# Optimization experiments

Hardware: AMD Instinct MI355X
Metric: run time of the kernel (lower is better)

The kernel has to match this reference:

```python
import jax, jax.numpy as jnp
import numpy as np

N = 50000      # nodes
E = 800000     # edges (avg degree 16)
IN, HID, OUT = 128, 256, 64
G = 500        # graphs in the batch (100 nodes each)
NEG_SLOPE = 0.01
EPS = 1e-12


def setup_inputs() -> dict:
    key = jax.random.key(0)
    ks = jax.random.split(key, 9)
    x = jax.random.normal(ks[0], (N, IN), jnp.float32)
    edge_index = jax.random.randint(ks[1], (2, E), 0, N, dtype=jnp.int32)
    # sorted segment ids with every graph present (100 nodes per graph)
    batch = jnp.repeat(jnp.arange(G, dtype=jnp.int32), N // G)
    def lin(k, fan_in, fan_out):
        s = 1.0 / np.sqrt(fan_in)
        kw, kb = jax.random.split(k)
        W = jax.random.uniform(kw, (fan_in, fan_out), jnp.float32, -s, s)
        b = jax.random.uniform(kb, (fan_out,), jnp.float32, -s, s)
        return W, b
    W1, b1 = lin(ks[2], IN, HID)
    W2, b2 = lin(ks[3], HID, HID)
    W3, b3 = lin(ks[4], HID, OUT)
    return {"x": x, "edge_index": edge_index, "batch": batch,
            "W1": W1, "b1": b1, "W2": W2, "b2": b2, "W3": W3, "b3": b3}


def _sage_conv(x, edge_index, W, b):
    # SAGEConv(aggr='add', root_weight=False, normalize=True):
    # gather source features, scatter-add to targets, linear, L2 normalize.
    src, dst = edge_index[0], edge_index[1]
    agg = jax.ops.segment_sum(x[src], dst, num_segments=x.shape[0])  # [N, d_in]
    out = agg @ W + b                                                 # [N, d_out]
    nrm = jnp.linalg.norm(out, axis=-1, keepdims=True)
    return out / jnp.maximum(nrm, EPS)


def reference(x, edge_index, batch, W1, b1, W2, b2, W3, b3):
    h = _sage_conv(x, edge_index, W1, b1)
    h = jax.nn.leaky_relu(h, NEG_SLOPE)          # dropout p=0 -> identity
    h = _sage_conv(h, edge_index, W2, b2)
    h = jax.nn.leaky_relu(h, NEG_SLOPE)
    h = _sage_conv(h, edge_index, W3, b3)
    # get_zero_nodes: first node of each graph (batch sorted, all G present)
    mask = jnp.concatenate([jnp.ones((1,), bool), batch[1:] != batch[:-1]])
    first_idx = jnp.nonzero(mask, size=G)[0]
    return h[first_idx]                          # [G, OUT]
```

## Files before the change

kernel.cpp:

```cpp
#include <hip/hip_runtime.h>

#define N_NODES 50000
#define E_EDGES 800000
#define IN_DIM  128
#define HID_DIM 256
#define OUT_DIM 64
#define G_GRAPHS 500
#define CAP 64
#define NBINS 196
#define BINCAP 5120

typedef __attribute__((ext_vector_type(8))) short short8;
typedef __attribute__((ext_vector_type(4))) float float4v;

__device__ __forceinline__ float bf2f(unsigned short u) {
  union { unsigned int i; float f; } c; c.i = ((unsigned int)u) << 16; return c.f;
}
__device__ __forceinline__ unsigned short f2bf(float f) {
  union { float f; unsigned int i; } c; c.f = f;
  unsigned int x = c.i;
  x += 0x7FFFu + ((x >> 16) & 1u);
  return (unsigned short)(x >> 16);
}
__device__ __forceinline__ unsigned int fbits(float f) {
  union { float f; unsigned int i; } c; c.f = f; return c.i;
}
__device__ __forceinline__ float bits2f(unsigned int u) {
  union { unsigned int i; float f; } c; c.i = u; return c.f;
}


__global__ __launch_bounds__(256) void prep1(
    const int* __restrict__ src, const int* __restrict__ dst,
    const int* __restrict__ batch,
    const float* __restrict__ x,
    const float* __restrict__ W1, const float* __restrict__ W2,
    unsigned int* __restrict__ binbuf, int* __restrict__ bin_next,
    int* __restrict__ first_node, unsigned char* __restrict__ is_first,
    unsigned short* __restrict__ xb,
    unsigned short* __restrict__ W1t, unsigned short* __restrict__ W2t) {
  const int b = blockIdx.x, tid = threadIdx.x;
  if (b < 200) {
    __shared__ int cnt[NBINS];
    __shared__ int gbase[NBINS];
    for (int i = tid; i < NBINS; i += 256) cnt[i] = 0;
    __syncthreads();
    const int base = b * 4096;
    unsigned int pk[16]; int bp[16];
#pragma unroll
    for (int u = 0; u < 16; ++u) {
      const int e = base + u * 256 + tid;
      bp[u] = -1;
      if (e < E_EDGES) {
        const int d = dst[e];
        const int s = src[e];
        const int bin = d >> 8;
        const int pos = atomicAdd(&cnt[bin], 1);
        pk[u] = ((unsigned int)(d & 255) << 16) | (unsigned int)s;
        bp[u] = (bin << 16) | pos;
      }
    }
    __syncthreads();
    for (int i = tid; i < NBINS; i += 256)
      gbase[i] = atomicAdd(&bin_next[i], cnt[i]);
    __syncthreads();
#pragma unroll
    for (int u = 0; u < 16; ++u) {
      if (bp[u] >= 0) {
        const int bin = bp[u] >> 16, pos = bp[u] & 0xFFFF;
        const int idx = gbase[bin] + pos;
        if (idx < BINCAP) binbuf[bin * BINCAP + idx] = pk[u];
      }
    }
  } else if (b < 6450) {
    const int t = (b - 200) * 256 + tid;
    const int i = t * 4;
    const float4 v = *(const float4*)(x + i);
    ushort4 u;
    u.x = f2bf(v.x); u.y = f2bf(v.y); u.z = f2bf(v.z); u.w = f2bf(v.w);
    *(ushort4*)(xb + i) = u;
    if (t < N_NODES) {
      const int fl = (t == 0 || batch[t] != batch[t - 1]) ? 1 : 0;
      is_first[t] = (unsigned char)fl;
      if (fl) first_node[batch[t]] = t;
    }
  } else {
    const int t = (b - 6450) * 256 + tid;
    if (t < 8192) {
      const int n = t >> 5, k0 = (t & 31) * 4;
      ushort4 o;
      o.x = f2bf(W1[(k0 + 0) * 256 + n]);
      o.y = f2bf(W1[(k0 + 1) * 256 + n]);
      o.z = f2bf(W1[(k0 + 2) * 256 + n]);
      o.w = f2bf(W1[(k0 + 3) * 256 + n]);
      *(ushort4*)&W1t[n * 128 + k0] = o;
    } else {
      const int v2 = t - 8192;
      const int n = v2 >> 6, k0 = (v2 & 63) * 4;
      ushort4 o;
      o.x = f2bf(W2[(k0 + 0) * 256 + n]);
      o.y = f2bf(W2[(k0 + 1) * 256 + n]);
      o.z = f2bf(W2[(k0 + 2) * 256 + n]);
      o.w = f2bf(W2[(k0 + 3) * 256 + n]);
      *(ushort4*)&W2t[n * 256 + k0] = o;
    }
  }
}


__global__ __launch_bounds__(512) void prep2(
    const unsigned int* __restrict__ binbuf, const int* __restrict__ bin_next,
    const unsigned char* __restrict__ is_first,
    int* __restrict__ deg, unsigned short* __restrict__ srcs,
    int* __restrict__ list2, int* __restrict__ cnt2) {
  __shared__ unsigned short img[256 * CAP];
  __shared__ int cnt[256];
  const int tid = threadIdx.x;
  const int bin = blockIdx.x;
  if (tid < 256) cnt[tid] = 0;
  __syncthreads();
  const int total = min(bin_next[bin], BINCAP);
  const unsigned int* bb = binbuf + bin * BINCAP;
  for (int i = tid; i < total; i += 512) {
    const unsigned int pk = bb[i];
    const int nl = pk >> 16;
    const int pos = atomicAdd(&cnt[nl], 1);
    if (pos < CAP) img[(nl << 6) + pos] = (unsigned short)(pk & 0xFFFFu);
  }
  __syncthreads();
  const int node0 = bin << 8;
  const int nend = min(N_NODES, node0 + 256);
  if (tid < 256 && node0 + tid < nend) {
    const int c = min(cnt[tid], CAP);
    deg[node0 + tid] = cnt[tid];
    if (is_first[node0 + tid]) {
      const int base = atomicAdd(cnt2, c);
      for (int q = 0; q < c; ++q) list2[base + q] = (int)img[(tid << 6) + q];
    }
  }
  const int nwords = (nend - node0) * 32;
  unsigned int* dstw = (unsigned int*)(srcs + ((size_t)node0 << 6));
  const unsigned int* srcw = (const unsigned int*)img;
  for (int i = tid; i < nwords; i += 512) dstw[i] = srcw[i];
}


template<int K, bool LIST>
__global__ __launch_bounds__(512, 8) void fused_layer(
    const unsigned short* __restrict__ H,
    const int* __restrict__ deg, const unsigned short* __restrict__ srcs,
    const unsigned short* __restrict__ Wt,
    const float* __restrict__ bias,
    unsigned short* __restrict__ Hout,
    const int* __restrict__ nodelist,
    const int* __restrict__ pcount)
{
  constexpr int M = 256;
  constexpr int TN = 16;
  constexpr int VPT = K / 64;
  constexpr int LDK = K + 8;
  __shared__ unsigned short a_hi[TN][LDK];
  __shared__ unsigned short a_lo[TN][LDK];
  __shared__ float ssq_tot[TN];
  __shared__ int nid_s[TN];
  const int tid = threadIdx.x;
  const int lane = tid & 63;
  const int wv = tid >> 6;

  int total = N_NODES;
  if constexpr (LIST) {
    total = __builtin_amdgcn_readfirstlane(*pcount);
    if (blockIdx.x * TN >= total) return;
  }

  if (tid < TN) {
    int gi = blockIdx.x * TN + tid;
    if constexpr (LIST) {
      if (gi >= total) gi = total - 1;
      nid_s[tid] = nodelist[gi];
    } else {
      nid_s[tid] = gi;
    }
    ssq_tot[tid] = 0.f;
  }
  __syncthreads();

  const unsigned short* hb = H + lane * VPT;
  const int node0 = __builtin_amdgcn_readfirstlane(nid_s[2 * wv]);
  const int node1 = __builtin_amdgcn_readfirstlane(nid_s[2 * wv + 1]);
  const int cnt0 = __builtin_amdgcn_readfirstlane(min(deg[node0], CAP));
  const int cnt1 = __builtin_amdgcn_readfirstlane(min(deg[node1], CAP));
  int idx0 = 0, idx1 = 0;
  if (lane < cnt0) idx0 = srcs[(node0 << 6) + lane];
  if (lane < cnt1) idx1 = srcs[(node1 << 6) + lane];

  float acc0[VPT], acc1[VPT];
#pragma unroll
  for (int q = 0; q < VPT; ++q) { acc0[q] = 0.f; acc1[q] = 0.f; }
  int j0 = 0, j1 = 0;

  if constexpr (VPT == 2) {
    while (j0 + 16 <= cnt0 && j1 + 16 <= cnt1) {
      int s0[16], s1[16];
#pragma unroll
      for (int u = 0; u < 16; ++u) {
        s0[u] = __builtin_amdgcn_readlane(idx0, j0 + u);
        s1[u] = __builtin_amdgcn_readlane(idx1, j1 + u);
      }
      ushort2 r0[16], r1[16];
#pragma unroll
      for (int u = 0; u < 16; ++u) r0[u] = *(const ushort2*)(hb + s0[u] * K);
#pragma unroll
      for (int u = 0; u < 16; ++u) r1[u] = *(const ushort2*)(hb + s1[u] * K);
#pragma unroll
      for (int u = 0; u < 16; ++u) {
        acc0[0] += bf2f(r0[u].x); acc0[1] += bf2f(r0[u].y);
        acc1[0] += bf2f(r1[u].x); acc1[1] += bf2f(r1[u].y);
      }
      j0 += 16; j1 += 16;
    }
  }

#pragma unroll
  for (int i = 0; i < 2; ++i) {
    const int nn = 2 * wv + i;
    const int cnt = i ? cnt1 : cnt0;
    const int idx = i ? idx1 : idx0;
    float (&acc)[VPT] = i ? acc1 : acc0;
    int j = i ? j1 : j0;

    for (; j + 16 <= cnt; j += 16) {
      int s[16];
#pragma unroll
      for (int u = 0; u < 16; ++u) s[u] = __builtin_amdgcn_readlane(idx, j + u);
      if constexpr (VPT == 4) {
        ushort4 r[16];
#pragma unroll
        for (int u = 0; u < 16; ++u) r[u] = *(const ushort4*)(hb + s[u] * K);
#pragma unroll
        for (int u = 0; u < 16; ++u) {
          acc[0] += bf2f(r[u].x); acc[1] += bf2f(r[u].y);
          acc[2] += bf2f(r[u].z); acc[3] += bf2f(r[u].w);
        }
      } else {
        ushort2 r[16];
#pragma unroll
        for (int u = 0; u < 16; ++u) r[u] = *(const ushort2*)(hb + s[u] * K);
#pragma unroll
        for (int u = 0; u < 16; ++u) {
          acc[0] += bf2f(r[u].x); acc[1] += bf2f(r[u].y);
        }
      }
    }
    for (; j < cnt; j += 8) {
      int s[8]; float w[8];
#pragma unroll
      for (int u = 0; u < 8; ++u) {
        const int q = j + u;
        const int qm = (q < cnt) ? q : (cnt - 1);
        s[u] = __builtin_amdgcn_readlane(idx, qm);
        w[u] = (q < cnt) ? 1.f : 0.f;
      }
      if constexpr (VPT == 4) {
        ushort4 r[8];
#pragma unroll
        for (int u = 0; u < 8; ++u) r[u] = *(const ushort4*)(hb + s[u] * K);
#pragma unroll
        for (int u = 0; u < 8; ++u) {
          acc[0] = fmaf(w[u], bf2f(r[u].x), acc[0]);
          acc[1] = fmaf(w[u], bf2f(r[u].y), acc[1]);
          acc[2] = fmaf(w[u], bf2f(r[u].z), acc[2]);
          acc[3] = fmaf(w[u], bf2f(r[u].w), acc[3]);
        }
      } else {
        ushort2 r[8];
#pragma unroll
        for (int u = 0; u < 8; ++u) r[u] = *(const ushort2*)(hb + s[u] * K);
#pragma unroll
        for (int u = 0; u < 8; ++u) {
          acc[0] = fmaf(w[u], bf2f(r[u].x), acc[0]);
          acc[1] = fmaf(w[u], bf2f(r[u].y), acc[1]);
        }
      }
    }

    unsigned short h[VPT], l[VPT];
#pragma unroll
    for (int jj = 0; jj < VPT; ++jj) {
      const unsigned int u = fbits(acc[jj]);
      h[jj] = (unsigned short)(u >> 16);
      const float res = acc[jj] - bits2f(u & 0xFFFF0000u);
      l[jj] = (unsigned short)(fbits(res) >> 16);
    }
    if constexpr (VPT == 4) {
      *(ushort4*)&a_hi[nn][lane * 4] = make_ushort4(h[0], h[1], h[2], h[3]);
      *(ushort4*)&a_lo[nn][lane * 4] = make_ushort4(l[0], l[1], l[2], l[3]);
    } else {
      *(ushort2*)&a_hi[nn][lane * 2] = make_ushort2(h[0], h[1]);
      *(ushort2*)&a_lo[nn][lane * 2] = make_ushort2(l[0], l[1]);
    }
  }
  __syncthreads();

  const int g = lane >> 4;
  const int lc = lane & 15;
  float4v dacc0 = (float4v){0.f, 0.f, 0.f, 0.f};
  float4v dacc1 = (float4v){0.f, 0.f, 0.f, 0.f};
  const unsigned short* W0 = Wt + (size_t)(wv * 16 + lc) * K + g * 8;
  const unsigned short* W1r = Wt + (size_t)((wv + 8) * 16 + lc) * K + g * 8;
#pragma unroll
  for (int ks = 0; ks < K / 32; ++ks) {
    const short8 ah = *(const short8*)&a_hi[lc][ks * 32 + g * 8];
    const short8 al = *(const short8*)&a_lo[lc][ks * 32 + g * 8];
    const short8 b0 = *(const short8*)(W0 + ks * 32);
    const short8 b1 = *(const short8*)(W1r + ks * 32);
    dacc0 = __builtin_amdgcn_mfma_f32_16x16x32_bf16(ah, b0, dacc0, 0, 0, 0);
    dacc0 = __builtin_amdgcn_mfma_f32_16x16x32_bf16(al, b0, dacc0, 0, 0, 0);
    dacc1 = __builtin_amdgcn_mfma_f32_16x16x32_bf16(ah, b1, dacc1, 0, 0, 0);
    dacc1 = __builtin_amdgcn_mfma_f32_16x16x32_bf16(al, b1, dacc1, 0, 0, 0);
  }

  const float bn0 = bias[wv * 16 + lc];
  const float bn1 = bias[(wv + 8) * 16 + lc];
  float4v o0 = dacc0 + bn0;
  float4v o1 = dacc1 + bn1;
  float sq[4];
#pragma unroll
  for (int r = 0; r < 4; ++r) sq[r] = o0[r] * o0[r] + o1[r] * o1[r];
#pragma unroll
  for (int off = 1; off < 16; off <<= 1) {
#pragma unroll
    for (int r = 0; r < 4; ++r) sq[r] += __shfl_xor(sq[r], off);
  }
  if (lc == 0) {
#pragma unroll
    for (int r = 0; r < 4; ++r) atomicAdd(&ssq_tot[g * 4 + r], sq[r]);
  }
  __syncthreads();

#pragma unroll
  for (int r = 0; r < 4; ++r) {
    const float inv = 1.f / fmaxf(sqrtf(ssq_tot[g * 4 + r]), 1e-12f);
    float v0 = o0[r] * inv;
    float v1 = o1[r] * inv;
    v0 = (v0 >= 0.f) ? v0 : 0.01f * v0;
    v1 = (v1 >= 0.f) ? v1 : 0.01f * v1;
    const int nd = nid_s[g * 4 + r];
    Hout[(size_t)nd * M + wv * 16 + lc] = f2bf(v0);
    Hout[(size_t)nd * M + (wv + 8) * 16 + lc] = f2bf(v1);
  }
}


__global__ __launch_bounds__(64) void layer3_kernel(
    const unsigned short* __restrict__ H2,
    const int* __restrict__ deg, const unsigned short* __restrict__ srcs,
    const int* __restrict__ first_node,
    const float* __restrict__ W,
    const float* __restrict__ bias,
    float* __restrict__ out)
{
  __shared__ float a_s[HID_DIM];
  const int g = blockIdx.x;
  const int lane = threadIdx.x;
  const int node = first_node[g];
  const int cnt = min(deg[node], CAP);
  float acc[4] = {0.f, 0.f, 0.f, 0.f};
  for (int p = 0; p < cnt; ++p) {
    const int s = srcs[(node << 6) + p];
    const ushort4 u = *(const ushort4*)(H2 + (size_t)s * HID_DIM + lane * 4);
    acc[0] += bf2f(u.x); acc[1] += bf2f(u.y); acc[2] += bf2f(u.z); acc[3] += bf2f(u.w);
  }
  *(float4*)&a_s[lane * 4] = make_float4(acc[0], acc[1], acc[2], acc[3]);
  __syncthreads();
  float o = bias[lane];
#pragma unroll 8
  for (int k = 0; k < HID_DIM; ++k) o += a_s[k] * W[k * OUT_DIM + lane];
  float ss = o * o;
#pragma unroll
  for (int off = 32; off > 0; off >>= 1) ss += __shfl_xor(ss, off);
  const float inv = 1.f / fmaxf(sqrtf(ss), 1e-12f);
  out[(size_t)g * OUT_DIM + lane] = o * inv;
}


extern "C" void kernel_launch(void* const* d_in, const int* in_sizes, int n_in,
                              void* d_out, int out_size, void* d_ws, size_t ws_size,
                              hipStream_t stream) {
  (void)in_sizes; (void)n_in; (void)out_size; (void)ws_size;
  const float* x   = (const float*)d_in[0];
  const int* ei    = (const int*)d_in[1];
  const int* batch = (const int*)d_in[2];
  const float* W1  = (const float*)d_in[3];
  const float* b1  = (const float*)d_in[4];
  const float* W2  = (const float*)d_in[5];
  const float* b2  = (const float*)d_in[6];
  const float* W3  = (const float*)d_in[7];
  const float* b3  = (const float*)d_in[8];
  const int* src = ei;
  const int* dst = ei + E_EDGES;

  char* ws = (char*)d_ws;
  size_t off = 0;
  auto alloc = [&](size_t bytes) {
    void* p = ws + off;
    off = (off + bytes + 255) & ~(size_t)255;
    return p;
  };
  int* cnts    = (int*)alloc(256);
  int* bin_next= (int*)alloc((size_t)NBINS * 4);
  const size_t zero_len = off;
  int* cnt2 = cnts;

  int* deg    = (int*)alloc((size_t)N_NODES * 4);
  unsigned short* srcs = (unsigned short*)alloc((size_t)N_NODES * CAP * 2);
  int* first  = (int*)alloc((size_t)G_GRAPHS * 4);
  unsigned char* is_first = (unsigned char*)alloc((size_t)N_NODES);
  int* list2  = (int*)alloc((size_t)G_GRAPHS * CAP * 4);
  unsigned int* binbuf = (unsigned int*)alloc((size_t)NBINS * BINCAP * 4);
  unsigned short* W1t = (unsigned short*)alloc((size_t)256 * 128 * 2);
  unsigned short* W2t = (unsigned short*)alloc((size_t)256 * 256 * 2);
  unsigned short* h2 = (unsigned short*)alloc((size_t)N_NODES * HID_DIM * 2);
  unsigned short* xb = h2;
  unsigned short* h1 = (unsigned short*)alloc((size_t)N_NODES * HID_DIM * 2);

  hipMemsetAsync(cnts, 0, zero_len, stream);

  prep1<<<6546, 256, 0, stream>>>(src, dst, batch, x, W1, W2,
                                  binbuf, bin_next, first, is_first, xb, W1t, W2t);
  prep2<<<NBINS, 512, 0, stream>>>(binbuf, bin_next, is_first, deg, srcs, list2, cnt2);

  fused_layer<IN_DIM, false><<<N_NODES / 16, 512, 0, stream>>>(
      xb, deg, srcs, W1t, b1, h1, nullptr, nullptr);
  fused_layer<HID_DIM, true><<<(G_GRAPHS * CAP) / 16, 512, 0, stream>>>(
      h1, deg, srcs, W2t, b2, h2, list2, cnt2);
  layer3_kernel<<<G_GRAPHS, 64, 0, stream>>>(h2, deg, srcs, first, W3, b3, (float*)d_out);
}
```

Before: 197.1 us.

## Replace atomic edge binning with per-block sort and fuse layer-3 aggregation into layer 2

Edge binning no longer uses global atomic bin counters or a memset. Each block sorts its own edge chunk by bin in shared memory and publishes prefix offsets, which prep2 reads back per bin. Layer 2 now runs four blocks per graph over that graph's first-node neighbour slots and writes per-graph partial sums of the activated outputs, so h2 is never stored or re-gathered. Layer 3 only adds the four partials. This removes a memset launch, global atomics and a gather pass, at the cost of a prefix-scan inside prep1 and some idle lanes for padded neighbour slots.

```diff
diff --git a/kernel.cpp b/kernel.cpp
--- a/kernel.cpp
+++ b/kernel.cpp
@@ -8,7 +8,7 @@
 #define G_GRAPHS 500
 #define CAP 64
 #define NBINS 196
-#define BINCAP 5120
+#define NEB   200
 
 typedef __attribute__((ext_vector_type(8))) short short8;
 typedef __attribute__((ext_vector_type(4))) float float4v;
@@ -35,15 +35,18 @@
     const int* __restrict__ batch,
     const float* __restrict__ x,
     const float* __restrict__ W1, const float* __restrict__ W2,
-    unsigned int* __restrict__ binbuf, int* __restrict__ bin_next,
-    int* __restrict__ first_node, unsigned char* __restrict__ is_first,
+    unsigned int* __restrict__ gout,
+    unsigned short* __restrict__ pref,
+    unsigned char* __restrict__ is_first,
     unsigned short* __restrict__ xb,
     unsigned short* __restrict__ W1t, unsigned short* __restrict__ W2t) {
+  __shared__ unsigned int s_sorted[4096];
+  __shared__ int s_cnt[256];
+  __shared__ int s_pa[256];
+  __shared__ int s_pb[256];
   const int b = blockIdx.x, tid = threadIdx.x;
-  if (b < 200) {
-    __shared__ int cnt[NBINS];
-    __shared__ int gbase[NBINS];
-    for (int i = tid; i < NBINS; i += 256) cnt[i] = 0;
+  if (b < NEB) {
+    s_cnt[tid] = 0;
     __syncthreads();
     const int base = b * 4096;
     unsigned int pk[16]; int bp[16];
@@ -55,34 +58,42 @@
         const int d = dst[e];
         const int s = src[e];
         const int bin = d >> 8;
-        const int pos = atomicAdd(&cnt[bin], 1);
+        const int r = atomicAdd(&s_cnt[bin], 1);
         pk[u] = ((unsigned int)(d & 255) << 16) | (unsigned int)s;
-        bp[u] = (bin << 16) | pos;
+        bp[u] = (bin << 16) | r;
       }
     }
     __syncthreads();
-    for (int i = tid; i < NBINS; i += 256)
-      gbase[i] = atomicAdd(&bin_next[i], cnt[i]);
+    const int v = s_cnt[tid];
+    s_pa[tid] = v;
     __syncthreads();
+    for (int st = 1; st < 256; st <<= 1) {
+      const int t = (tid >= st) ? s_pa[tid - st] : 0;
+      __syncthreads();
+      s_pa[tid] += t;
+      __syncthreads();
+    }
+    const int excl = s_pa[tid] - v;
+    s_pb[tid] = excl;
+    pref[(b << 8) + tid] = (unsigned short)excl;
+    __syncthreads();
 #pragma unroll
     for (int u = 0; u < 16; ++u) {
-      if (bp[u] >= 0) {
-        const int bin = bp[u] >> 16, pos = bp[u] & 0xFFFF;
-        const int idx = gbase[bin] + pos;
-        if (idx < BINCAP) binbuf[bin * BINCAP + idx] = pk[u];
-      }
-    }
+      if (bp[u] >= 0)
+        s_sorted[s_pb[bp[u] >> 16] + (bp[u] & 0xFFFF)] = pk[u];
+    }
+    __syncthreads();
+    const int nb = s_pa[255];
+    for (int i = tid; i < nb; i += 256) gout[base + i] = s_sorted[i];
   } else if (b < 6450) {
-    const int t = (b - 200) * 256 + tid;
+    const int t = (b - NEB) * 256 + tid;
     const int i = t * 4;
     const float4 v = *(const float4*)(x + i);
     ushort4 u;
     u.x = f2bf(v.x); u.y = f2bf(v.y); u.z = f2bf(v.z); u.w = f2bf(v.w);
     *(ushort4*)(xb + i) = u;
     if (t < N_NODES) {
-      const int fl = (t == 0 || batch[t] != batch[t - 1]) ? 1 : 0;
-      is_first[t] = (unsigned char)fl;
-      if (fl) first_node[batch[t]] = t;
+      is_first[t] = (t == 0 || batch[t] != batch[t - 1]) ? 1 : 0;
     }
   } else {
     const int t = (b - 6450) * 256 + tid;
@@ -109,33 +120,47 @@
 
 
 __global__ __launch_bounds__(512) void prep2(
-    const unsigned int* __restrict__ binbuf, const int* __restrict__ bin_next,
-    const unsigned char* __restrict__ is_first,
+    const unsigned int* __restrict__ gout, const unsigned short* __restrict__ pref,
+    const int* __restrict__ batch, const unsigned char* __restrict__ is_first,
     int* __restrict__ deg, unsigned short* __restrict__ srcs,
-    int* __restrict__ list2, int* __restrict__ cnt2) {
+    unsigned short* __restrict__ list2, int* __restrict__ l2cnt) {
   __shared__ unsigned short img[256 * CAP];
   __shared__ int cnt[256];
+  __shared__ unsigned short st_s[NEB], ln_s[NEB];
   const int tid = threadIdx.x;
   const int bin = blockIdx.x;
   if (tid < 256) cnt[tid] = 0;
-  __syncthreads();
-  const int total = min(bin_next[bin], BINCAP);
-  const unsigned int* bb = binbuf + bin * BINCAP;
-  for (int i = tid; i < total; i += 512) {
-    const unsigned int pk = bb[i];
-    const int nl = pk >> 16;
-    const int pos = atomicAdd(&cnt[nl], 1);
-    if (pos < CAP) img[(nl << 6) + pos] = (unsigned short)(pk & 0xFFFFu);
+  if (tid < NEB) {
+    const unsigned short a = pref[(tid << 8) + bin];
+    const unsigned short e = pref[(tid << 8) + bin + 1];
+    st_s[tid] = a; ln_s[tid] = (unsigned short)(e - a);
+  }
+  __syncthreads();
+  const int wv = tid >> 6, lane = tid & 63;
+  for (int bb = wv; bb < NEB; bb += 8) {
+    const int len = ln_s[bb];
+    const int go = bb * 4096 + st_s[bb];
+    for (int base = 0; base < len; base += 64) {
+      if (base + lane < len) {
+        const unsigned int pk = gout[go + base + lane];
+        const int nl = pk >> 16;
+        const int pos = atomicAdd(&cnt[nl], 1);
+        if (pos < CAP) img[(nl << 6) + pos] = (unsigned short)(pk & 0xFFFFu);
+      }
+    }
   }
   __syncthreads();
   const int node0 = bin << 8;
   const int nend = min(N_NODES, node0 + 256);
   if (tid < 256 && node0 + tid < nend) {
-    const int c = min(cnt[tid], CAP);
-    deg[node0 + tid] = cnt[tid];
+    const int c = cnt[tid];
+    deg[node0 + tid] = c;
     if (is_first[node0 + tid]) {
-      const int base = atomicAdd(cnt2, c);
-      for (int q = 0; q < c; ++q) list2[base + q] = (int)img[(tid << 6) + q];
+      const int g = batch[node0 + tid];
+      l2cnt[g] = min(c, CAP);
+      unsigned int* d = (unsigned int*)(list2 + g * 64);
+      const unsigned int* s = (const unsigned int*)(img + (tid << 6));
+      for (int q = 0; q < 32; ++q) d[q] = s[q];
     }
   }
   const int nwords = (nend - node0) * 32;
@@ -145,15 +170,16 @@
 }
 
 
-template<int K, bool LIST>
+template<int K, int MODE>
 __global__ __launch_bounds__(512, 8) void fused_layer(
     const unsigned short* __restrict__ H,
     const int* __restrict__ deg, const unsigned short* __restrict__ srcs,
     const unsigned short* __restrict__ Wt,
     const float* __restrict__ bias,
     unsigned short* __restrict__ Hout,
-    const int* __restrict__ nodelist,
-    const int* __restrict__ pcount)
+    const unsigned short* __restrict__ list2,
+    const int* __restrict__ l2cnt,
+    float* __restrict__ agg_part)
 {
   constexpr int M = 256;
   constexpr int TN = 16;
@@ -162,24 +188,23 @@
   __shared__ unsigned short a_hi[TN][LDK];
   __shared__ unsigned short a_lo[TN][LDK];
   __shared__ float ssq_tot[TN];
+  __shared__ float vld_s[TN];
   __shared__ int nid_s[TN];
   const int tid = threadIdx.x;
   const int lane = tid & 63;
   const int wv = tid >> 6;
-
-  int total = N_NODES;
-  if constexpr (LIST) {
-    total = __builtin_amdgcn_readfirstlane(*pcount);
-    if (blockIdx.x * TN >= total) return;
-  }
+  const int graph = blockIdx.x >> 2;
+  const int p = blockIdx.x & 3;
 
   if (tid < TN) {
-    int gi = blockIdx.x * TN + tid;
-    if constexpr (LIST) {
-      if (gi >= total) gi = total - 1;
-      nid_s[tid] = nodelist[gi];
+    if constexpr (MODE == 1) {
+      const int slot = p * 16 + tid;
+      const bool vld = slot < l2cnt[graph];
+      nid_s[tid] = vld ? (int)list2[graph * 64 + slot] : 0;
+      vld_s[tid] = vld ? 1.f : 0.f;
     } else {
-      nid_s[tid] = gi;
+      nid_s[tid] = blockIdx.x * TN + tid;
+      vld_s[tid] = 1.f;
     }
     ssq_tot[tid] = 0.f;
   }
@@ -188,8 +213,12 @@
   const unsigned short* hb = H + lane * VPT;
   const int node0 = __builtin_amdgcn_readfirstlane(nid_s[2 * wv]);
   const int node1 = __builtin_amdgcn_readfirstlane(nid_s[2 * wv + 1]);
-  const int cnt0 = __builtin_amdgcn_readfirstlane(min(deg[node0], CAP));
-  const int cnt1 = __builtin_amdgcn_readfirstlane(min(deg[node1], CAP));
+  int cnt0 = __builtin_amdgcn_readfirstlane(min(deg[node0], CAP));
+  int cnt1 = __builtin_amdgcn_readfirstlane(min(deg[node1], CAP));
+  if constexpr (MODE == 1) {
+    if (vld_s[2 * wv] == 0.f) cnt0 = 0;
+    if (vld_s[2 * wv + 1] == 0.f) cnt1 = 0;
+  }
   int idx0 = 0, idx1 = 0;
   if (lane < cnt0) idx0 = srcs[(node0 << 6) + lane];
   if (lane < cnt1) idx1 = srcs[(node1 << 6) + lane];
@@ -338,24 +367,43 @@
   }
   __syncthreads();
 
-#pragma unroll
-  for (int r = 0; r < 4; ++r) {
-    const float inv = 1.f / fmaxf(sqrtf(ssq_tot[g * 4 + r]), 1e-12f);
-    float v0 = o0[r] * inv;
-    float v1 = o1[r] * inv;
-    v0 = (v0 >= 0.f) ? v0 : 0.01f * v0;
-    v1 = (v1 >= 0.f) ? v1 : 0.01f * v1;
-    const int nd = nid_s[g * 4 + r];
-    Hout[(size_t)nd * M + wv * 16 + lc] = f2bf(v0);
-    Hout[(size_t)nd * M + (wv + 8) * 16 + lc] = f2bf(v1);
+  if constexpr (MODE == 0) {
+#pragma unroll
+    for (int r = 0; r < 4; ++r) {
+      const float inv = 1.f / fmaxf(sqrtf(ssq_tot[g * 4 + r]), 1e-12f);
+      float v0 = o0[r] * inv;
+      float v1 = o1[r] * inv;
+      v0 = (v0 >= 0.f) ? v0 : 0.01f * v0;
+      v1 = (v1 >= 0.f) ? v1 : 0.01f * v1;
+      const int nd = nid_s[g * 4 + r];
+      Hout[(size_t)nd * M + wv * 16 + lc] = f2bf(v0);
+      Hout[(size_t)nd * M + (wv + 8) * 16 + lc] = f2bf(v1);
+    }
+  } else {
+    float s0 = 0.f, s1 = 0.f;
+#pragma unroll
+    for (int r = 0; r < 4; ++r) {
+      const float inv = 1.f / fmaxf(sqrtf(ssq_tot[g * 4 + r]), 1e-12f);
+      float v0 = o0[r] * inv;
+      float v1 = o1[r] * inv;
+      v0 = (v0 >= 0.f) ? v0 : 0.01f * v0;
+      v1 = (v1 >= 0.f) ? v1 : 0.01f * v1;
+      const float w = vld_s[g * 4 + r];
+      s0 += w * v0; s1 += w * v1;
+    }
+    s0 += __shfl_xor(s0, 16); s0 += __shfl_xor(s0, 32);
+    s1 += __shfl_xor(s1, 16); s1 += __shfl_xor(s1, 32);
+    if (lane < 16) {
+      float* pp = agg_part + ((size_t)(graph * 4 + p) << 8);
+      pp[wv * 16 + lane] = s0;
+      pp[128 + wv * 16 + lane] = s1;
+    }
   }
 }
 
 
 __global__ __launch_bounds__(64) void layer3_kernel(
-    const unsigned short* __restrict__ H2,
-    const int* __restrict__ deg, const unsigned short* __restrict__ srcs,
-    const int* __restrict__ first_node,
+    const float* __restrict__ agg_part,
     const float* __restrict__ W,
     const float* __restrict__ bias,
     float* __restrict__ out)
@@ -363,15 +411,12 @@
   __shared__ float a_s[HID_DIM];
   const int g = blockIdx.x;
   const int lane = threadIdx.x;
-  const int node = first_node[g];
-  const int cnt = min(deg[node], CAP);
-  float acc[4] = {0.f, 0.f, 0.f, 0.f};
-  for (int p = 0; p < cnt; ++p) {
-    const int s = srcs[(node << 6) + p];
-    const ushort4 u = *(const ushort4*)(H2 + (size_t)s * HID_DIM + lane * 4);
-    acc[0] += bf2f(u.x); acc[1] += bf2f(u.y); acc[2] += bf2f(u.z); acc[3] += bf2f(u.w);
-  }
-  *(float4*)&a_s[lane * 4] = make_float4(acc[0], acc[1], acc[2], acc[3]);
+  const float* pp = agg_part + ((size_t)g << 10);
+#pragma unroll
+  for (int c = 0; c < 4; ++c) {
+    const int idx = c * 64 + lane;
+    a_s[idx] = pp[idx] + pp[256 + idx] + pp[512 + idx] + pp[768 + idx];
+  }
   __syncthreads();
   float o = bias[lane];
 #pragma unroll 8
@@ -407,32 +452,27 @@
     off = (off + bytes + 255) & ~(size_t)255;
     return p;
   };
-  int* cnts    = (int*)alloc(256);
-  int* bin_next= (int*)alloc((size_t)NBINS * 4);
-  const size_t zero_len = off;
-  int* cnt2 = cnts;
-
   int* deg    = (int*)alloc((size_t)N_NODES * 4);
   unsigned short* srcs = (unsigned short*)alloc((size_t)N_NODES * CAP * 2);
-  int* first  = (int*)alloc((size_t)G_GRAPHS * 4);
   unsigned char* is_first = (unsigned char*)alloc((size_t)N_NODES);
-  int* list2  = (int*)alloc((size_t)G_GRAPHS * CAP * 4);
-  unsigned int* binbuf = (unsigned int*)alloc((size_t)NBINS * BINCAP * 4);
+  unsigned short* list2 = (unsigned short*)alloc((size_t)G_GRAPHS * CAP * 2);
+  int* l2cnt  = (int*)alloc((size_t)G_GRAPHS * 4);
+  unsigned int* gout = (unsigned int*)alloc((size_t)NEB * 4096 * 4);
+  unsigned short* pref = (unsigned short*)alloc((size_t)NEB * 256 * 2);
+  float* agg_part = (float*)alloc((size_t)G_GRAPHS * 4 * 256 * 4);
   unsigned short* W1t = (unsigned short*)alloc((size_t)256 * 128 * 2);
   unsigned short* W2t = (unsigned short*)alloc((size_t)256 * 256 * 2);
-  unsigned short* h2 = (unsigned short*)alloc((size_t)N_NODES * HID_DIM * 2);
-  unsigned short* xb = h2;
+  unsigned short* xb = (unsigned short*)alloc((size_t)N_NODES * IN_DIM * 2);
   unsigned short* h1 = (unsigned short*)alloc((size_t)N_NODES * HID_DIM * 2);
 
-  hipMemsetAsync(cnts, 0, zero_len, stream);
-
   prep1<<<6546, 256, 0, stream>>>(src, dst, batch, x, W1, W2,
-                                  binbuf, bin_next, first, is_first, xb, W1t, W2t);
-  prep2<<<NBINS, 512, 0, stream>>>(binbuf, bin_next, is_first, deg, srcs, list2, cnt2);
-
-  fused_layer<IN_DIM, false><<<N_NODES / 16, 512, 0, stream>>>(
-      xb, deg, srcs, W1t, b1, h1, nullptr, nullptr);
-  fused_layer<HID_DIM, true><<<(G_GRAPHS * CAP) / 16, 512, 0, stream>>>(
-      h1, deg, srcs, W2t, b2, h2, list2, cnt2);
-  layer3_kernel<<<G_GRAPHS, 64, 0, stream>>>(h2, deg, srcs, first, W3, b3, (float*)d_out);
-}
+                                  gout, pref, is_first, xb, W1t, W2t);
+  prep2<<<NBINS, 512, 0, stream>>>(gout, pref, batch, is_first, deg, srcs,
+                                   list2, l2cnt);
+
+  fused_layer<IN_DIM, 0><<<N_NODES / 16, 512, 0, stream>>>(
+      xb, deg, srcs, W1t, b1, h1, nullptr, nullptr, nullptr);
+  fused_layer<HID_DIM, 1><<<G_GRAPHS * 4, 512, 0, stream>>>(
+      h1, deg, srcs, W2t, b2, nullptr, list2, l2cnt, agg_part);
+  layer3_kernel<<<G_GRAPHS, 64, 0, stream>>>(agg_part, W3, b3, (float*)d_out);
+}
```

After: 223.8 us. +13.5%, slower.
